# Kernel tuning notes

Hardware: AMD Instinct MI355X
Metric: run time of the kernel (lower is better)

## Reference

```python
import jax, jax.numpy as jnp
import numpy as np

ATT_SCALE = 1.0

def setup_inputs() -> dict:
    key = jax.random.key(0)
    ks = jax.random.split(key, 9)
    N, Cin, Cout, E = 50000, 512, 512, 400000
    x = jax.random.normal(ks[0], (N, Cin), dtype=jnp.float32)
    eb = jax.random.randint(ks[1], (2, E), 0, N, dtype=jnp.int32)
    ev = jax.random.randint(ks[2], (2, E), 0, N, dtype=jnp.int32)
    ec = jax.random.randint(ks[3], (2, E), 0, N, dtype=jnp.int32)
    s = 1.0 / np.sqrt(Cin)
    W_bond = jax.random.normal(ks[4], (Cout, Cin), dtype=jnp.float32) * s
    W_vin = jax.random.normal(ks[5], (Cout, Cin), dtype=jnp.float32) * s
    W_vconn = jax.random.normal(ks[6], (Cout, Cin), dtype=jnp.float32) * s
    att_proj = jax.random.normal(ks[7], (Cout,), dtype=jnp.float32)
    bias = jnp.zeros((Cout,), dtype=jnp.float32)
    return {"x": x, "edge_index_bond": eb, "edge_index_virtual_intra": ev,
            "edge_index_virtual_conn": ec, "W_bond": W_bond, "W_vin": W_vin,
            "W_vconn": W_vconn, "att_proj": att_proj, "bias": bias}

def reference(x, edge_index_bond, edge_index_virtual_intra, edge_index_virtual_conn,
              W_bond, W_vin, W_vconn, att_proj, bias):
    N = x.shape[0]
    x_bond = x @ W_bond.T    # [N, Cout]
    x_vin = x @ W_vin.T
    x_vconn = x @ W_vconn.T

    # --- bond edges: add self loops, symmetric degree normalization ---
    loops = jnp.arange(N, dtype=edge_index_bond.dtype)
    row = jnp.concatenate([edge_index_bond[0], loops])
    col = jnp.concatenate([edge_index_bond[1], loops])
    deg = jax.ops.segment_sum(jnp.ones_like(row, dtype=x_bond.dtype), row, num_segments=N)
    dinv = jnp.where(deg > 0, deg ** -0.5, 0.0)
    norm = dinv[row] * dinv[col]                       # [E+N]
    out = jax.ops.segment_sum(x_bond[col] * norm[:, None], row, num_segments=N)

    # --- virtual intra edges: mean aggregation ---
    row_v, col_v = edge_index_virtual_intra[0], edge_index_virtual_intra[1]
    sum_vin = jax.ops.segment_sum(x_vin[col_v], row_v, num_segments=N)
    deg_vin = jnp.clip(jax.ops.segment_sum(jnp.ones_like(row_v, dtype=x_vin.dtype), row_v, num_segments=N), 1.0)
    out = out + sum_vin / deg_vin[:, None]

    # --- virtual conn edges: sigmoid dot-product attention ---
    row_c, col_c = edge_index_virtual_conn[0], edge_index_virtual_conn[1]
    proj_i = x_vconn[row_c] * att_proj
    proj_j = x_vconn[col_c] * att_proj
    alpha = jax.nn.sigmoid(jnp.sum(proj_i * proj_j, axis=-1) * ATT_SCALE)  # [E]
    out = out + jax.ops.segment_sum(alpha[:, None] * x_vconn[col_c], row_c, num_segments=N)

    return out + bias
```

## Files before the change

kernel.cpp:

```cpp
#include <hip/hip_runtime.h>
#include <stdint.h>

typedef _Float16 f16x8 __attribute__((ext_vector_type(8)));
typedef _Float16 f16x2 __attribute__((ext_vector_type(2)));
typedef float f32x4 __attribute__((ext_vector_type(4)));

__device__ __forceinline__ unsigned short f2h(float f) {
    _Float16 h = (_Float16)f;
    return __builtin_bit_cast(unsigned short, h);
}
__device__ __forceinline__ float h2f(unsigned short s) {
    _Float16 h = __builtin_bit_cast(_Float16, s);
    return (float)h;
}

__device__ __forceinline__ void gload16(const void* g, void* lds) {
    __builtin_amdgcn_global_load_lds(
        (const __attribute__((address_space(1))) void*)g,
        (__attribute__((address_space(3))) void*)lds, 16, 0, 0);
}

#if __has_builtin(__builtin_amdgcn_fdot2)
__device__ __forceinline__ float dot2(f16x2 a, f16x2 b, float c) {
    return __builtin_amdgcn_fdot2(a, b, c, false);
}
#else
__device__ __forceinline__ float dot2(f16x2 a, f16x2 b, float c) {
    return c + (float)a[0] * (float)b[0] + (float)a[1] * (float)b[1];
}
#endif

__global__ __launch_bounds__(256) void k_convert_w(
    const float* __restrict__ Wb, const float* __restrict__ Wv,
    const float* __restrict__ Wc, unsigned short* __restrict__ Wf)
{
    int idx = blockIdx.x * 256 + threadIdx.x;
    if (idx >= 1536 * 512) return;
    int m = idx >> 9, k = idx & 511;
    float s;
    if (m < 512)       s = Wb[m * 512 + k];
    else if (m < 1024) s = Wv[(m - 512) * 512 + k];
    else               s = Wc[(m - 1024) * 512 + k];
    Wf[idx] = f2h(s);
}

__global__ __launch_bounds__(256) void k_conv_x(
    const float* __restrict__ x, unsigned short* __restrict__ xf,
    size_t valid, size_t total)
{
    size_t idx = ((size_t)blockIdx.x * 256 + threadIdx.x) * 4;
    if (idx >= total) return;
    ushort4 h;
    if (idx < valid) {
        float4 f = *(const float4*)(x + idx);
        h.x = f2h(f.x); h.y = f2h(f.y); h.z = f2h(f.z); h.w = f2h(f.w);
    } else {
        h.x = h.y = h.z = h.w = 0;
    }
    *(ushort4*)(xf + idx) = h;
}

__global__ __launch_bounds__(256) void k_hist3(
    const int* __restrict__ eb, const int* __restrict__ ev, const int* __restrict__ ec,
    int Eb, int Ev, int Ec, int* __restrict__ cnt, int N)
{
    int i = blockIdx.x * 256 + threadIdx.x;
    if (i < Eb) atomicAdd(cnt + eb[i], 1);
    else if (i < Eb + Ev) atomicAdd(cnt + N + ev[i - Eb], 1);
    else if (i < Eb + Ev + Ec) atomicAdd(cnt + 2 * N + ec[i - Eb - Ev], 1);
}

__global__ __launch_bounds__(256) void k_scan_a(
    const int* __restrict__ cnt, int* __restrict__ ptr, int* __restrict__ bsum, int M)
{
    __shared__ int sh[256];
    int t = threadIdx.x;
    int base = blockIdx.x * 1024 + t * 4;
    int v[4];
    #pragma unroll
    for (int j = 0; j < 4; j++) v[j] = (base + j < M) ? cnt[base + j] : 0;
    int local = v[0] + v[1] + v[2] + v[3];
    sh[t] = local; __syncthreads();
    #pragma unroll
    for (int off = 1; off < 256; off <<= 1) {
        int x = (t >= off) ? sh[t - off] : 0;
        __syncthreads();
        sh[t] += x;
        __syncthreads();
    }
    int run = sh[t] - local;
    #pragma unroll
    for (int j = 0; j < 4; j++) {
        if (base + j < M) ptr[base + j] = run;
        run += v[j];
    }
    if (t == 255) bsum[blockIdx.x] = sh[255];
}

__global__ __launch_bounds__(256) void k_scan_b(int* __restrict__ bsum, int nb)
{
    __shared__ int sh[256];
    int t = threadIdx.x;
    int v = (t < nb) ? bsum[t] : 0;
    sh[t] = v; __syncthreads();
    #pragma unroll
    for (int off = 1; off < 256; off <<= 1) {
        int x = (t >= off) ? sh[t - off] : 0;
        __syncthreads();
        sh[t] += x;
        __syncthreads();
    }
    if (t < nb) bsum[t] = sh[t] - v;
}

__global__ __launch_bounds__(256) void k_scan_c(
    int* __restrict__ ptr, const int* __restrict__ bsum, int* __restrict__ cur,
    const int* __restrict__ cnt, float* __restrict__ dinv,
    int M, int N, int total)
{
    int idx = blockIdx.x * 256 + threadIdx.x;
    if (idx < M) {
        int p = ptr[idx] + bsum[idx >> 10];
        ptr[idx] = p;
        cur[idx] = p;
        if (idx < N) dinv[idx] = rsqrtf((float)(cnt[idx] + 1));
    }
    if (idx == 0) ptr[M] = total;
}

__global__ __launch_bounds__(256) void k_scatter3(
    const int* __restrict__ eb, const int* __restrict__ ev, const int* __restrict__ ec,
    int Eb, int Ev, int Ec, int* __restrict__ cur, int* __restrict__ cidx, int N)
{
    int i = blockIdx.x * 256 + threadIdx.x;
    const int* e; int il, off, E;
    if (i < Eb) { e = eb; il = i; off = 0; E = Eb; }
    else if (i < Eb + Ev) { e = ev; il = i - Eb; off = N; E = Ev; }
    else if (i < Eb + Ev + Ec) { e = ec; il = i - Eb - Ev; off = 2 * N; E = Ec; }
    else return;
    int r = e[il], c = e[E + il];
    int pos = atomicAdd(cur + off + r, 1);
    cidx[pos] = c;
}

__global__ __launch_bounds__(256) void k_gemm_f(
    const unsigned short* __restrict__ xf, const unsigned short* __restrict__ Wf,
    unsigned short* __restrict__ Ybv, unsigned short* __restrict__ Ycf)
{
    __shared__ uint4 As[1024];
    __shared__ uint4 Bs[1024];

    const int id = blockIdx.x;
    const int xcd = id & 7;
    const int jj = id >> 3;
    const int bn = jj % 12;
    const int bm = xcd + 8 * (jj / 12);

    const int t = threadIdx.x;
    const int lane = t & 63;
    const int w = t >> 6;
    const int wr = w >> 1, wc = w & 1;
    const int rA = lane >> 3;
    const int cs = lane & 7;

    f32x4 acc[4][4];
    #pragma unroll
    for (int i = 0; i < 4; i++)
        #pragma unroll
        for (int j = 0; j < 4; j++) acc[i][j] = (f32x4){0.f, 0.f, 0.f, 0.f};

    const size_t baseA = (size_t)bm * 128 * 512;
    const size_t baseB = (size_t)bn * 128 * 512;

    for (int kt = 0; kt < 512; kt += 64) {
        #pragma unroll
        for (int j = 0; j < 4; j++) {
            int seg = w * 4 + j;
            int r = seg * 8 + rA;
            int cg = cs ^ (r & 7);
            gload16(xf + baseA + (size_t)r * 512 + kt + cg * 8, &As[seg * 64]);
            gload16(Wf + baseB + (size_t)r * 512 + kt + cg * 8, &Bs[seg * 64]);
        }
        __syncthreads();
        #pragma unroll
        for (int kk = 0; kk < 2; kk++) {
            f16x8 a[4], b[4];
            #pragma unroll
            for (int ni = 0; ni < 4; ni++) {
                int ar = wr * 64 + ni * 16 + (lane & 15);
                int k8 = kk * 4 + (lane >> 4);
                a[ni] = __builtin_bit_cast(f16x8, As[ar * 8 + (k8 ^ (ar & 7))]);
            }
            #pragma unroll
            for (int mi = 0; mi < 4; mi++) {
                int br = wc * 64 + mi * 16 + (lane & 15);
                int k8 = kk * 4 + (lane >> 4);
                b[mi] = __builtin_bit_cast(f16x8, Bs[br * 8 + (k8 ^ (br & 7))]);
            }
            #pragma unroll
            for (int mi = 0; mi < 4; mi++)
                #pragma unroll
                for (int ni = 0; ni < 4; ni++)
                    acc[mi][ni] = __builtin_amdgcn_mfma_f32_16x16x32_f16(
                        a[ni], b[mi], acc[mi][ni], 0, 0, 0);
        }
        __syncthreads();
    }

    const int nbase = bm * 128 + wr * 64 + (lane >> 4) * 4;
    const int mbase = bn * 128 + wc * 64 + (lane & 15);
    if (bn < 8) {
        #pragma unroll
        for (int mi = 0; mi < 4; mi++) {
            int m = mbase + mi * 16;
            #pragma unroll
            for (int ni = 0; ni < 4; ni++) {
                int n0 = nbase + ni * 16;
                #pragma unroll
                for (int j = 0; j < 4; j++)
                    Ybv[(size_t)(n0 + j) * 1024 + m] = f2h(acc[mi][ni][j]);
            }
        }
    } else {
        #pragma unroll
        for (int mi = 0; mi < 4; mi++) {
            int m = mbase + mi * 16 - 1024;
            #pragma unroll
            for (int ni = 0; ni < 4; ni++) {
                int n0 = nbase + ni * 16;
                #pragma unroll
                for (int j = 0; j < 4; j++)
                    Ycf[(size_t)(n0 + j) * 512 + m] = f2h(acc[mi][ni][j]);
            }
        }
    }
}

__device__ __forceinline__ void acc_h8(float* a, uint4 v, float s) {
    a[0] += s * h2f((unsigned short)(v.x & 0xffff));
    a[1] += s * h2f((unsigned short)(v.x >> 16));
    a[2] += s * h2f((unsigned short)(v.y & 0xffff));
    a[3] += s * h2f((unsigned short)(v.y >> 16));
    a[4] += s * h2f((unsigned short)(v.z & 0xffff));
    a[5] += s * h2f((unsigned short)(v.z >> 16));
    a[6] += s * h2f((unsigned short)(v.w & 0xffff));
    a[7] += s * h2f((unsigned short)(v.w >> 16));
}
__device__ __forceinline__ float dot8(const f16x2* ph, uint4 u) {
    float d = 0.f;
    d = dot2(ph[0], __builtin_bit_cast(f16x2, u.x), d);
    d = dot2(ph[1], __builtin_bit_cast(f16x2, u.y), d);
    d = dot2(ph[2], __builtin_bit_cast(f16x2, u.z), d);
    d = dot2(ph[3], __builtin_bit_cast(f16x2, u.w), d);
    return d;
}

__global__ __launch_bounds__(256) void k_gather(
    const int* __restrict__ ptr, const int* __restrict__ cidx,
    const float* __restrict__ dinv,
    const unsigned short* __restrict__ Ybv, const unsigned short* __restrict__ Ycf,
    const float* __restrict__ att, const float* __restrict__ bias,
    float* __restrict__ out, int N)
{
    int node = blockIdx.x * 4 + (threadIdx.x >> 6);
    if (node >= N) return;
    int lane = threadIdx.x & 63;

    float a[8];
    {
        const float4* bp = (const float4*)(bias + lane * 8);
        float4 q0 = bp[0], q1 = bp[1];
        a[0] = q0.x; a[1] = q0.y; a[2] = q0.z; a[3] = q0.w;
        a[4] = q1.x; a[5] = q1.y; a[6] = q1.z; a[7] = q1.w;
    }

    float di = dinv[node];
    {
        uint4 v = *((const uint4*)(Ybv + (size_t)node * 1024) + lane);
        acc_h8(a, v, di * di);
    }
    {
        int e0 = ptr[node], e1 = ptr[node + 1];
        int e = e0;
        for (; e + 4 <= e1; e += 4) {
            int c0 = cidx[e], c1 = cidx[e + 1], c2 = cidx[e + 2], c3 = cidx[e + 3];
            uint4 v0 = *((const uint4*)(Ybv + (size_t)c0 * 1024) + lane);
            uint4 v1 = *((const uint4*)(Ybv + (size_t)c1 * 1024) + lane);
            uint4 v2 = *((const uint4*)(Ybv + (size_t)c2 * 1024) + lane);
            uint4 v3 = *((const uint4*)(Ybv + (size_t)c3 * 1024) + lane);
            float n0 = di * dinv[c0], n1 = di * dinv[c1];
            float n2 = di * dinv[c2], n3 = di * dinv[c3];
            acc_h8(a, v0, n0); acc_h8(a, v1, n1);
            acc_h8(a, v2, n2); acc_h8(a, v3, n3);
        }
        for (; e < e1; ++e) {
            int c = cidx[e];
            uint4 v = *((const uint4*)(Ybv + (size_t)c * 1024) + lane);
            acc_h8(a, v, di * dinv[c]);
        }
    }
    {
        int e0 = ptr[N + node], e1 = ptr[N + node + 1];
        float vsc = 1.0f / (float)((e1 - e0) > 1 ? (e1 - e0) : 1);
        int e = e0;
        for (; e + 4 <= e1; e += 4) {
            int c0 = cidx[e], c1 = cidx[e + 1], c2 = cidx[e + 2], c3 = cidx[e + 3];
            uint4 v0 = *((const uint4*)(Ybv + (size_t)c0 * 1024 + 512) + lane);
            uint4 v1 = *((const uint4*)(Ybv + (size_t)c1 * 1024 + 512) + lane);
            uint4 v2 = *((const uint4*)(Ybv + (size_t)c2 * 1024 + 512) + lane);
            uint4 v3 = *((const uint4*)(Ybv + (size_t)c3 * 1024 + 512) + lane);
            acc_h8(a, v0, vsc); acc_h8(a, v1, vsc);
            acc_h8(a, v2, vsc); acc_h8(a, v3, vsc);
        }
        for (; e < e1; ++e) {
            int c = cidx[e];
            uint4 v = *((const uint4*)(Ybv + (size_t)c * 1024 + 512) + lane);
            acc_h8(a, v, vsc);
        }
    }
    {
        int e0 = ptr[2 * N + node], e1 = ptr[2 * N + node + 1];
        if (e0 < e1) {
            const float4* ap = (const float4*)att + lane * 2;
            float4 t0 = ap[0], t1 = ap[1];
            float yr[8];
            {
                uint4 u = *((const uint4*)(Ycf + (size_t)node * 512) + lane);
                yr[0] = h2f((unsigned short)(u.x & 0xffff));
                yr[1] = h2f((unsigned short)(u.x >> 16));
                yr[2] = h2f((unsigned short)(u.y & 0xffff));
                yr[3] = h2f((unsigned short)(u.y >> 16));
                yr[4] = h2f((unsigned short)(u.z & 0xffff));
                yr[5] = h2f((unsigned short)(u.z >> 16));
                yr[6] = h2f((unsigned short)(u.w & 0xffff));
                yr[7] = h2f((unsigned short)(u.w >> 16));
            }
            f16x2 ph[4];
            ph[0] = (f16x2){(_Float16)(yr[0] * t0.x * t0.x), (_Float16)(yr[1] * t0.y * t0.y)};
            ph[1] = (f16x2){(_Float16)(yr[2] * t0.z * t0.z), (_Float16)(yr[3] * t0.w * t0.w)};
            ph[2] = (f16x2){(_Float16)(yr[4] * t1.x * t1.x), (_Float16)(yr[5] * t1.y * t1.y)};
            ph[3] = (f16x2){(_Float16)(yr[6] * t1.z * t1.z), (_Float16)(yr[7] * t1.w * t1.w)};
            int e = e0;
            for (; e + 4 <= e1; e += 4) {
                int c0 = cidx[e], c1 = cidx[e + 1], c2 = cidx[e + 2], c3 = cidx[e + 3];
                uint4 u0 = *((const uint4*)(Ycf + (size_t)c0 * 512) + lane);
                uint4 u1 = *((const uint4*)(Ycf + (size_t)c1 * 512) + lane);
                uint4 u2 = *((const uint4*)(Ycf + (size_t)c2 * 512) + lane);
                uint4 u3 = *((const uint4*)(Ycf + (size_t)c3 * 512) + lane);
                float d0 = dot8(ph, u0);
                float d1 = dot8(ph, u1);
                float d2 = dot8(ph, u2);
                float d3 = dot8(ph, u3);
                #pragma unroll
                for (int off = 32; off > 0; off >>= 1) {
                    d0 += __shfl_xor(d0, off);
                    d1 += __shfl_xor(d1, off);
                    d2 += __shfl_xor(d2, off);
                    d3 += __shfl_xor(d3, off);
                }
                float al0 = 1.0f / (1.0f + expf(-d0));
                float al1 = 1.0f / (1.0f + expf(-d1));
                float al2 = 1.0f / (1.0f + expf(-d2));
                float al3 = 1.0f / (1.0f + expf(-d3));
                acc_h8(a, u0, al0); acc_h8(a, u1, al1);
                acc_h8(a, u2, al2); acc_h8(a, u3, al3);
            }
            for (; e < e1; ++e) {
                int c = cidx[e];
                uint4 u = *((const uint4*)(Ycf + (size_t)c * 512) + lane);
                float dot = dot8(ph, u);
                #pragma unroll
                for (int off = 32; off > 0; off >>= 1) dot += __shfl_xor(dot, off);
                float alpha = 1.0f / (1.0f + expf(-dot));
                acc_h8(a, u, alpha);
            }
        }
    }
    float4 o0 = make_float4(a[0], a[1], a[2], a[3]);
    float4 o1 = make_float4(a[4], a[5], a[6], a[7]);
    float4* dst = (float4*)(out + (size_t)node * 512 + lane * 8);
    dst[0] = o0; dst[1] = o1;
}

extern "C" void kernel_launch(void* const* d_in, const int* in_sizes, int n_in,
                              void* d_out, int out_size, void* d_ws, size_t ws_size,
                              hipStream_t stream) {
    const float* x    = (const float*)d_in[0];
    const int*   eb   = (const int*)d_in[1];
    const int*   ev   = (const int*)d_in[2];
    const int*   ec   = (const int*)d_in[3];
    const float* Wb   = (const float*)d_in[4];
    const float* Wv   = (const float*)d_in[5];
    const float* Wc   = (const float*)d_in[6];
    const float* att  = (const float*)d_in[7];
    const float* bias = (const float*)d_in[8];
    float* out = (float*)d_out;

    const int N  = in_sizes[0] / 512;
    const int Eb = in_sizes[1] / 2;
    const int Ev = in_sizes[2] / 2;
    const int Ec = in_sizes[3] / 2;
    const int Etot = Eb + Ev + Ec;
    const int nbm = (((N + 127) / 128 + 7) / 8) * 8;
    const size_t Npad = (size_t)nbm * 128;
    const int M = 3 * N;
    const int nScanBlocks = (M + 1023) / 1024;

    char* p = (char*)d_ws;
    unsigned short* Ybv = (unsigned short*)p; p += Npad * 1024 * 2;
    unsigned short* Ycf = (unsigned short*)p; p += Npad * 512 * 2;
    unsigned short* Wf  = (unsigned short*)p; p += (size_t)1536 * 512 * 2;
    unsigned short* xf  = (unsigned short*)p; p += Npad * 512 * 2;
    int* cnt  = (int*)p; p += ((size_t)M * 4 + 255) & ~(size_t)255;
    int* ptr_ = (int*)p; p += ((size_t)(M + 1) * 4 + 255) & ~(size_t)255;
    int* cur  = (int*)p; p += ((size_t)M * 4 + 255) & ~(size_t)255;
    int* bsum = (int*)p; p += 256 * 4;
    int* cidx = (int*)p; p += ((size_t)Etot * 4 + 255) & ~(size_t)255;
    float* dinv = (float*)p; p += ((size_t)N * 4 + 255) & ~(size_t)255;

    hipMemsetAsync(cnt, 0, (size_t)M * 4, stream);
    k_hist3<<<(Etot + 255) / 256, 256, 0, stream>>>(eb, ev, ec, Eb, Ev, Ec, cnt, N);
    k_scan_a<<<nScanBlocks, 256, 0, stream>>>(cnt, ptr_, bsum, M);
    k_scan_b<<<1, 256, 0, stream>>>(bsum, nScanBlocks);
    k_scan_c<<<(M + 255) / 256, 256, 0, stream>>>(ptr_, bsum, cur, cnt, dinv, M, N, Etot);
    k_scatter3<<<(Etot + 255) / 256, 256, 0, stream>>>(eb, ev, ec, Eb, Ev, Ec, cur, cidx, N);

    k_convert_w<<<(1536 * 512 + 255) / 256, 256, 0, stream>>>(Wb, Wv, Wc, Wf);
    {
        size_t total = Npad * 512, valid = (size_t)N * 512;
        k_conv_x<<<(int)((total / 4 + 255) / 256), 256, 0, stream>>>(x, xf, valid, total);
    }
    k_gemm_f<<<nbm * 12, 256, 0, stream>>>(xf, Wf, Ybv, Ycf);

    k_gather<<<(N + 3) / 4, 256, 0, stream>>>(ptr_, cidx, dinv, Ybv, Ycf, att, bias, out, N);
}
```

Before: 478.4 us.

## Split each node's edge gather across two wavefronts and reduce through LDS

The gather kernel now gives each node a 128-thread block of two wavefronts. Each wavefront processes half of the node's edges in all three edge sets, and the partial sums are combined through shared memory before the output is written. The aim is to double the memory-level parallelism per node and cut the per-wave serial latency over edge lists. The cost is a block barrier, an LDS round trip, duplicated query projection setup for the attention edges, and twice as many blocks. The output stores also switch to nontemporal.

```diff
diff --git a/kernel.cpp b/kernel.cpp
--- a/kernel.cpp
+++ b/kernel.cpp
@@ -255,32 +255,36 @@
     return d;
 }
 
-__global__ __launch_bounds__(256) void k_gather(
+__global__ __launch_bounds__(128) void k_gather(
     const int* __restrict__ ptr, const int* __restrict__ cidx,
     const float* __restrict__ dinv,
     const unsigned short* __restrict__ Ybv, const unsigned short* __restrict__ Ycf,
     const float* __restrict__ att, const float* __restrict__ bias,
     float* __restrict__ out, int N)
 {
-    int node = blockIdx.x * 4 + (threadIdx.x >> 6);
+    __shared__ float part[64][8];
+    int node = blockIdx.x;
     if (node >= N) return;
+    int wv = threadIdx.x >> 6;
     int lane = threadIdx.x & 63;
 
-    float a[8];
-    {
+    float a[8] = {0.f, 0.f, 0.f, 0.f, 0.f, 0.f, 0.f, 0.f};
+    float di = dinv[node];
+
+    if (wv == 0) {
         const float4* bp = (const float4*)(bias + lane * 8);
         float4 q0 = bp[0], q1 = bp[1];
         a[0] = q0.x; a[1] = q0.y; a[2] = q0.z; a[3] = q0.w;
         a[4] = q1.x; a[5] = q1.y; a[6] = q1.z; a[7] = q1.w;
-    }
-
-    float di = dinv[node];
-    {
         uint4 v = *((const uint4*)(Ybv + (size_t)node * 1024) + lane);
         acc_h8(a, v, di * di);
     }
+
     {
-        int e0 = ptr[node], e1 = ptr[node + 1];
+        int f0 = ptr[node], f1 = ptr[node + 1];
+        int half = (f1 - f0 + 1) >> 1;
+        int e0 = wv ? f0 + half : f0;
+        int e1 = wv ? f1 : f0 + half;
         int e = e0;
         for (; e + 4 <= e1; e += 4) {
             int c0 = cidx[e], c1 = cidx[e + 1], c2 = cidx[e + 2], c3 = cidx[e + 3];
@@ -300,8 +304,11 @@
         }
     }
     {
-        int e0 = ptr[N + node], e1 = ptr[N + node + 1];
-        float vsc = 1.0f / (float)((e1 - e0) > 1 ? (e1 - e0) : 1);
+        int f0 = ptr[N + node], f1 = ptr[N + node + 1];
+        float vsc = 1.0f / (float)((f1 - f0) > 1 ? (f1 - f0) : 1);
+        int half = (f1 - f0 + 1) >> 1;
+        int e0 = wv ? f0 + half : f0;
+        int e1 = wv ? f1 : f0 + half;
         int e = e0;
         for (; e + 4 <= e1; e += 4) {
             int c0 = cidx[e], c1 = cidx[e + 1], c2 = cidx[e + 2], c3 = cidx[e + 3];
@@ -319,7 +326,10 @@
         }
     }
     {
-        int e0 = ptr[2 * N + node], e1 = ptr[2 * N + node + 1];
+        int f0 = ptr[2 * N + node], f1 = ptr[2 * N + node + 1];
+        int half = (f1 - f0 + 1) >> 1;
+        int e0 = wv ? f0 + half : f0;
+        int e1 = wv ? f1 : f0 + half;
         if (e0 < e1) {
             const float4* ap = (const float4*)att + lane * 2;
             float4 t0 = ap[0], t1 = ap[1];
@@ -376,10 +386,21 @@
             }
         }
     }
-    float4 o0 = make_float4(a[0], a[1], a[2], a[3]);
-    float4 o1 = make_float4(a[4], a[5], a[6], a[7]);
-    float4* dst = (float4*)(out + (size_t)node * 512 + lane * 8);
-    dst[0] = o0; dst[1] = o1;
+
+    if (wv == 1) {
+        *(f32x4*)&part[lane][0] = (f32x4){a[0], a[1], a[2], a[3]};
+        *(f32x4*)&part[lane][4] = (f32x4){a[4], a[5], a[6], a[7]};
+    }
+    __syncthreads();
+    if (wv == 0) {
+        f32x4 p0 = *(f32x4*)&part[lane][0];
+        f32x4 p1 = *(f32x4*)&part[lane][4];
+        f32x4 o0 = (f32x4){a[0] + p0[0], a[1] + p0[1], a[2] + p0[2], a[3] + p0[3]};
+        f32x4 o1 = (f32x4){a[4] + p1[0], a[5] + p1[1], a[6] + p1[2], a[7] + p1[3]};
+        f32x4* dst = (f32x4*)(out + (size_t)node * 512 + lane * 8);
+        __builtin_nontemporal_store(o0, dst);
+        __builtin_nontemporal_store(o1, dst + 1);
+    }
 }
 
 extern "C" void kernel_launch(void* const* d_in, const int* in_sizes, int n_in,
@@ -432,5 +453,5 @@
     }
     k_gemm_f<<<nbm * 12, 256, 0, stream>>>(xf, Wf, Ybv, Ycf);
 
-    k_gather<<<(N + 3) / 4, 256, 0, stream>>>(ptr_, cidx, dinv, Ybv, Ycf, att, bias, out, N);
-}
+    k_gather<<<N, 128, 0, stream>>>(ptr_, cidx, dinv, Ybv, Ycf, att, bias, out, N);
+}
```

Measured after the change: 479.6 us. About the same (+0.2%).

## Fuse fp32-to-fp16 conversion of x into the GEMM A-tile load

Applied to the files above, without the earlier changes.

Removes the standalone x conversion kernel and its fp16 workspace. The GEMM now reads fp32 x directly, converts each A-tile to fp16 in registers and writes it to LDS. This also replaces the async global-to-LDS loads for A with synchronous register-staged loads. The final output store in the gather kernel switches to nontemporal stores. The intent is to save a full pass over x, at the cost of twice the bytes per A-tile load repeated across column blocks, and less load/compute overlap.

```diff
diff --git a/kernel.cpp b/kernel.cpp
--- a/kernel.cpp
+++ b/kernel.cpp
@@ -42,22 +42,6 @@
     else if (m < 1024) s = Wv[(m - 512) * 512 + k];
     else               s = Wc[(m - 1024) * 512 + k];
     Wf[idx] = f2h(s);
-}
-
-__global__ __launch_bounds__(256) void k_conv_x(
-    const float* __restrict__ x, unsigned short* __restrict__ xf,
-    size_t valid, size_t total)
-{
-    size_t idx = ((size_t)blockIdx.x * 256 + threadIdx.x) * 4;
-    if (idx >= total) return;
-    ushort4 h;
-    if (idx < valid) {
-        float4 f = *(const float4*)(x + idx);
-        h.x = f2h(f.x); h.y = f2h(f.y); h.z = f2h(f.z); h.w = f2h(f.w);
-    } else {
-        h.x = h.y = h.z = h.w = 0;
-    }
-    *(ushort4*)(xf + idx) = h;
 }
 
 __global__ __launch_bounds__(256) void k_hist3(
@@ -144,8 +128,8 @@
 }
 
 __global__ __launch_bounds__(256) void k_gemm_f(
-    const unsigned short* __restrict__ xf, const unsigned short* __restrict__ Wf,
-    unsigned short* __restrict__ Ybv, unsigned short* __restrict__ Ycf)
+    const float* __restrict__ x, const unsigned short* __restrict__ Wf,
+    unsigned short* __restrict__ Ybv, unsigned short* __restrict__ Ycf, int N)
 {
     __shared__ uint4 As[1024];
     __shared__ uint4 Bs[1024];
@@ -169,7 +153,6 @@
         #pragma unroll
         for (int j = 0; j < 4; j++) acc[i][j] = (f32x4){0.f, 0.f, 0.f, 0.f};
 
-    const size_t baseA = (size_t)bm * 128 * 512;
     const size_t baseB = (size_t)bn * 128 * 512;
 
     for (int kt = 0; kt < 512; kt += 64) {
@@ -177,9 +160,21 @@
         for (int j = 0; j < 4; j++) {
             int seg = w * 4 + j;
             int r = seg * 8 + rA;
-            int cg = cs ^ (r & 7);
-            gload16(xf + baseA + (size_t)r * 512 + kt + cg * 8, &As[seg * 64]);
+            int cg = cs ^ rA;
             gload16(Wf + baseB + (size_t)r * 512 + kt + cg * 8, &Bs[seg * 64]);
+            int ga = bm * 128 + r;
+            uint4 pk;
+            if (ga < N) {
+                const float4* ax = (const float4*)(x + (size_t)ga * 512 + kt + cg * 8);
+                float4 f0 = ax[0], f1 = ax[1];
+                pk.x = (unsigned)f2h(f0.x) | ((unsigned)f2h(f0.y) << 16);
+                pk.y = (unsigned)f2h(f0.z) | ((unsigned)f2h(f0.w) << 16);
+                pk.z = (unsigned)f2h(f1.x) | ((unsigned)f2h(f1.y) << 16);
+                pk.w = (unsigned)f2h(f1.z) | ((unsigned)f2h(f1.w) << 16);
+            } else {
+                pk.x = pk.y = pk.z = pk.w = 0u;
+            }
+            As[r * 8 + cs] = pk;
         }
         __syncthreads();
         #pragma unroll
@@ -376,10 +371,11 @@
             }
         }
     }
-    float4 o0 = make_float4(a[0], a[1], a[2], a[3]);
-    float4 o1 = make_float4(a[4], a[5], a[6], a[7]);
-    float4* dst = (float4*)(out + (size_t)node * 512 + lane * 8);
-    dst[0] = o0; dst[1] = o1;
+    f32x4 o0 = (f32x4){a[0], a[1], a[2], a[3]};
+    f32x4 o1 = (f32x4){a[4], a[5], a[6], a[7]};
+    f32x4* dst = (f32x4*)(out + (size_t)node * 512 + lane * 8);
+    __builtin_nontemporal_store(o0, dst);
+    __builtin_nontemporal_store(o1, dst + 1);
 }
 
 extern "C" void kernel_launch(void* const* d_in, const int* in_sizes, int n_in,
@@ -410,7 +406,6 @@
     unsigned short* Ybv = (unsigned short*)p; p += Npad * 1024 * 2;
     unsigned short* Ycf = (unsigned short*)p; p += Npad * 512 * 2;
     unsigned short* Wf  = (unsigned short*)p; p += (size_t)1536 * 512 * 2;
-    unsigned short* xf  = (unsigned short*)p; p += Npad * 512 * 2;
     int* cnt  = (int*)p; p += ((size_t)M * 4 + 255) & ~(size_t)255;
     int* ptr_ = (int*)p; p += ((size_t)(M + 1) * 4 + 255) & ~(size_t)255;
     int* cur  = (int*)p; p += ((size_t)M * 4 + 255) & ~(size_t)255;
@@ -426,11 +421,7 @@
     k_scatter3<<<(Etot + 255) / 256, 256, 0, stream>>>(eb, ev, ec, Eb, Ev, Ec, cur, cidx, N);
 
     k_convert_w<<<(1536 * 512 + 255) / 256, 256, 0, stream>>>(Wb, Wv, Wc, Wf);
-    {
-        size_t total = Npad * 512, valid = (size_t)N * 512;
-        k_conv_x<<<(int)((total / 4 + 255) / 256), 256, 0, stream>>>(x, xf, valid, total);
-    }
-    k_gemm_f<<<nbm * 12, 256, 0, stream>>>(xf, Wf, Ybv, Ycf);
+    k_gemm_f<<<nbm * 12, 256, 0, stream>>>(x, Wf, Ybv, Ycf, N);
 
     k_gather<<<(N + 3) / 4, 256, 0, stream>>>(ptr_, cidx, dinv, Ybv, Ycf, att, bias, out, N);
 }
```

Result: slower. 538.6 us (+12.6%).

## Fuse prep kernels, enlarge GEMM row tile to 256 with 8 waves, nontemporal output

Applied to the files above, without the earlier changes.

Merges the x conversion, weight conversion and edge histogram into one prep kernel, with the weight conversion vectorised to float4, so fewer launches are needed. The GEMM moves to 512-thread blocks covering 256 rows of x per block. B tiles are reused across twice as many rows, which cuts the number of blocks and the redundant weight loads, at the cost of more LDS per block. The gather's final output stores become nontemporal so they do not pollute the cache. Row padding grows to a multiple of 2048, and the prep kernel still covers the edge count only because that grid is much larger.

```diff
diff --git a/kernel.cpp b/kernel.cpp
--- a/kernel.cpp
+++ b/kernel.cpp
@@ -30,44 +30,43 @@
 }
 #endif
 
-__global__ __launch_bounds__(256) void k_convert_w(
+__global__ __launch_bounds__(256) void k_prep(
+    const float* __restrict__ x, unsigned short* __restrict__ xf,
+    size_t valid, size_t total,
     const float* __restrict__ Wb, const float* __restrict__ Wv,
-    const float* __restrict__ Wc, unsigned short* __restrict__ Wf)
-{
-    int idx = blockIdx.x * 256 + threadIdx.x;
-    if (idx >= 1536 * 512) return;
-    int m = idx >> 9, k = idx & 511;
-    float s;
-    if (m < 512)       s = Wb[m * 512 + k];
-    else if (m < 1024) s = Wv[(m - 512) * 512 + k];
-    else               s = Wc[(m - 1024) * 512 + k];
-    Wf[idx] = f2h(s);
-}
-
-__global__ __launch_bounds__(256) void k_conv_x(
-    const float* __restrict__ x, unsigned short* __restrict__ xf,
-    size_t valid, size_t total)
-{
-    size_t idx = ((size_t)blockIdx.x * 256 + threadIdx.x) * 4;
-    if (idx >= total) return;
-    ushort4 h;
-    if (idx < valid) {
-        float4 f = *(const float4*)(x + idx);
-        h.x = f2h(f.x); h.y = f2h(f.y); h.z = f2h(f.z); h.w = f2h(f.w);
-    } else {
-        h.x = h.y = h.z = h.w = 0;
-    }
-    *(ushort4*)(xf + idx) = h;
-}
-
-__global__ __launch_bounds__(256) void k_hist3(
+    const float* __restrict__ Wc, unsigned short* __restrict__ Wf,
     const int* __restrict__ eb, const int* __restrict__ ev, const int* __restrict__ ec,
     int Eb, int Ev, int Ec, int* __restrict__ cnt, int N)
 {
-    int i = blockIdx.x * 256 + threadIdx.x;
-    if (i < Eb) atomicAdd(cnt + eb[i], 1);
-    else if (i < Eb + Ev) atomicAdd(cnt + N + ev[i - Eb], 1);
-    else if (i < Eb + Ev + Ec) atomicAdd(cnt + 2 * N + ec[i - Eb - Ev], 1);
+    size_t i = (size_t)blockIdx.x * 256 + threadIdx.x;
+    size_t idx = i * 4;
+    if (idx < total) {
+        ushort4 h;
+        if (idx < valid) {
+            float4 f = *(const float4*)(x + idx);
+            h.x = f2h(f.x); h.y = f2h(f.y); h.z = f2h(f.z); h.w = f2h(f.w);
+        } else {
+            h.x = h.y = h.z = h.w = 0;
+        }
+        *(ushort4*)(xf + idx) = h;
+    }
+    if (idx < (size_t)1536 * 512) {
+        int m = (int)(idx >> 9), k = (int)(idx & 511);
+        const float* src;
+        if (m < 512)       src = Wb + (size_t)m * 512 + k;
+        else if (m < 1024) src = Wv + (size_t)(m - 512) * 512 + k;
+        else               src = Wc + (size_t)(m - 1024) * 512 + k;
+        float4 f = *(const float4*)src;
+        ushort4 h;
+        h.x = f2h(f.x); h.y = f2h(f.y); h.z = f2h(f.z); h.w = f2h(f.w);
+        *(ushort4*)(Wf + idx) = h;
+    }
+    if (i < (size_t)(Eb + Ev + Ec)) {
+        int ii = (int)i;
+        if (ii < Eb) atomicAdd(cnt + eb[ii], 1);
+        else if (ii < Eb + Ev) atomicAdd(cnt + N + ev[ii - Eb], 1);
+        else atomicAdd(cnt + 2 * N + ec[ii - Eb - Ev], 1);
+    }
 }
 
 __global__ __launch_bounds__(256) void k_scan_a(
@@ -143,11 +142,11 @@
     cidx[pos] = c;
 }
 
-__global__ __launch_bounds__(256) void k_gemm_f(
+__global__ __launch_bounds__(512) void k_gemm_f(
     const unsigned short* __restrict__ xf, const unsigned short* __restrict__ Wf,
     unsigned short* __restrict__ Ybv, unsigned short* __restrict__ Ycf)
 {
-    __shared__ uint4 As[1024];
+    __shared__ uint4 As[2048];
     __shared__ uint4 Bs[1024];
 
     const int id = blockIdx.x;
@@ -159,7 +158,8 @@
     const int t = threadIdx.x;
     const int lane = t & 63;
     const int w = t >> 6;
-    const int wr = w >> 1, wc = w & 1;
+    const int wr = w >> 1;
+    const int wc = w & 1;
     const int rA = lane >> 3;
     const int cs = lane & 7;
 
@@ -169,7 +169,7 @@
         #pragma unroll
         for (int j = 0; j < 4; j++) acc[i][j] = (f32x4){0.f, 0.f, 0.f, 0.f};
 
-    const size_t baseA = (size_t)bm * 128 * 512;
+    const size_t baseA = (size_t)bm * 256 * 512;
     const size_t baseB = (size_t)bn * 128 * 512;
 
     for (int kt = 0; kt < 512; kt += 64) {
@@ -177,8 +177,14 @@
         for (int j = 0; j < 4; j++) {
             int seg = w * 4 + j;
             int r = seg * 8 + rA;
-            int cg = cs ^ (r & 7);
+            int cg = cs ^ rA;
             gload16(xf + baseA + (size_t)r * 512 + kt + cg * 8, &As[seg * 64]);
+        }
+        #pragma unroll
+        for (int j = 0; j < 2; j++) {
+            int seg = w * 2 + j;
+            int r = seg * 8 + rA;
+            int cg = cs ^ rA;
             gload16(Wf + baseB + (size_t)r * 512 + kt + cg * 8, &Bs[seg * 64]);
         }
         __syncthreads();
@@ -207,7 +213,7 @@
         __syncthreads();
     }
 
-    const int nbase = bm * 128 + wr * 64 + (lane >> 4) * 4;
+    const int nbase = bm * 256 + wr * 64 + (lane >> 4) * 4;
     const int mbase = bn * 128 + wc * 64 + (lane & 15);
     if (bn < 8) {
         #pragma unroll
@@ -376,10 +382,11 @@
             }
         }
     }
-    float4 o0 = make_float4(a[0], a[1], a[2], a[3]);
-    float4 o1 = make_float4(a[4], a[5], a[6], a[7]);
-    float4* dst = (float4*)(out + (size_t)node * 512 + lane * 8);
-    dst[0] = o0; dst[1] = o1;
+    f32x4 o0 = (f32x4){a[0], a[1], a[2], a[3]};
+    f32x4 o1 = (f32x4){a[4], a[5], a[6], a[7]};
+    f32x4* dst = (f32x4*)(out + (size_t)node * 512 + lane * 8);
+    __builtin_nontemporal_store(o0, dst);
+    __builtin_nontemporal_store(o1, dst + 1);
 }
 
 extern "C" void kernel_launch(void* const* d_in, const int* in_sizes, int n_in,
@@ -401,8 +408,8 @@
     const int Ev = in_sizes[2] / 2;
     const int Ec = in_sizes[3] / 2;
     const int Etot = Eb + Ev + Ec;
-    const int nbm = (((N + 127) / 128 + 7) / 8) * 8;
-    const size_t Npad = (size_t)nbm * 128;
+    const int nbm = (((N + 255) / 256 + 7) / 8) * 8;
+    const size_t Npad = (size_t)nbm * 256;
     const int M = 3 * N;
     const int nScanBlocks = (M + 1023) / 1024;
 
@@ -418,19 +425,18 @@
     int* cidx = (int*)p; p += ((size_t)Etot * 4 + 255) & ~(size_t)255;
     float* dinv = (float*)p; p += ((size_t)N * 4 + 255) & ~(size_t)255;
 
+    const size_t total = Npad * 512, valid = (size_t)N * 512;
+
     hipMemsetAsync(cnt, 0, (size_t)M * 4, stream);
-    k_hist3<<<(Etot + 255) / 256, 256, 0, stream>>>(eb, ev, ec, Eb, Ev, Ec, cnt, N);
+    k_prep<<<(int)((total / 4 + 255) / 256), 256, 0, stream>>>(
+        x, xf, valid, total, Wb, Wv, Wc, Wf, eb, ev, ec, Eb, Ev, Ec, cnt, N);
+
     k_scan_a<<<nScanBlocks, 256, 0, stream>>>(cnt, ptr_, bsum, M);
     k_scan_b<<<1, 256, 0, stream>>>(bsum, nScanBlocks);
     k_scan_c<<<(M + 255) / 256, 256, 0, stream>>>(ptr_, bsum, cur, cnt, dinv, M, N, Etot);
     k_scatter3<<<(Etot + 255) / 256, 256, 0, stream>>>(eb, ev, ec, Eb, Ev, Ec, cur, cidx, N);
 
-    k_convert_w<<<(1536 * 512 + 255) / 256, 256, 0, stream>>>(Wb, Wv, Wc, Wf);
-    {
-        size_t total = Npad * 512, valid = (size_t)N * 512;
-        k_conv_x<<<(int)((total / 4 + 255) / 256), 256, 0, stream>>>(x, xf, valid, total);
-    }
-    k_gemm_f<<<nbm * 12, 256, 0, stream>>>(xf, Wf, Ybv, Ycf);
+    k_gemm_f<<<nbm * 12, 512, 0, stream>>>(xf, Wf, Ybv, Ycf);
 
     k_gather<<<(N + 3) / 4, 256, 0, stream>>>(ptr_, cidx, dinv, Ybv, Ycf, att, bias, out, N);
 }
```

Result: no change. 476.4 us (-0.4%).
